# Kernel optimization log

Hardware: AMD Instinct MI355X
Metric: run time of the kernel (lower is better)

Reference implementation:

```python
import jax, jax.numpy as jnp
import numpy as np
import math

B, H, N, DH = 4, 8, 1024, 128
DPT = 4  # point feature dim (<=4 branch: squared-distance map only)

def setup_inputs() -> dict:
    key = jax.random.key(0)
    ks = jax.random.split(key, 10)
    q   = jax.random.normal(ks[0], (B, H, N, DH), jnp.float32)
    k   = jax.random.normal(ks[1], (B, H, N, DH), jnp.float32)
    v   = jax.random.normal(ks[2], (B, H, N, DH), jnp.float32)
    c   = jax.random.normal(ks[3], (B, H, N, 1), jnp.float32)
    d_q = jax.random.normal(ks[4], (B, N, DPT), jnp.float32)
    d_k = jax.random.normal(ks[5], (B, N, DPT), jnp.float32)
    # LazyLinear(1 -> nhead): per-head scalar weight + bias
    w_w = jax.random.normal(ks[6], (H,), jnp.float32) * 0.1
    b_w = jax.random.normal(ks[7], (H,), jnp.float32) * 0.1
    w_b = jax.random.normal(ks[8], (H,), jnp.float32) * 0.1
    b_b = jax.random.normal(ks[9], (H,), jnp.float32) * 0.1
    return {"q": q, "k": k, "v": v, "c": c, "d_q": d_q, "d_k": d_k,
            "w_w": w_w, "b_w": b_w, "w_b": w_b, "b_b": b_b}

def reference(q, k, v, c, d_q, d_k, w_w, b_w, w_b, b_b):
    dh = q.shape[-1]
    # pairwise squared distances on first 3 coords (torch: under no_grad)
    dq3 = d_q[:, :, :3]
    dk3 = d_k[:, :, :3]
    dist = jax.lax.stop_gradient(
        jnp.sum(dq3 ** 2, -1)[:, :, None]
        + jnp.sum(dk3 ** 2, -1)[:, None, :]
        - 2.0 * jnp.einsum('bnd,bmd->bnm', dq3, dk3))  # [B,N,M]
    db = dist[:, None, :, :]  # [B,1,N,M]
    wbc = lambda p: p[None, :, None, None]  # [1,H,1,1]
    # distmap_w = softplus(-(w*dist + b)); distmap_b = w*dist + b (identity acts)
    distmap_w = jax.nn.softplus(-(db * wbc(w_w) + wbc(b_w)))  # [B,H,N,M]
    distmap_b = db * wbc(w_b) + wbc(b_b)                      # [B,H,N,M]
    # scaled dot-product scores per head
    scores = jnp.einsum('bhnd,bhmd->bhnm', q, k) / math.sqrt(dh)
    scores = jax.nn.relu(scores * distmap_w + distmap_b)
    detr = (jnp.sum(scores, -1, keepdims=True)
            + jnp.sum(jax.nn.softplus(c), 2, keepdims=True) + 1e-9)
    scores = scores / detr
    out = jnp.einsum('bhnm,bhmd->bhnd', scores, v)
    return out, scores
```

## Files before the change

### kernel.cpp

```cpp
#include <hip/hip_runtime.h>


typedef __attribute__((ext_vector_type(8))) short short8;
typedef __attribute__((ext_vector_type(4))) float f32x4;

#define OUT_ELEMS 4194304ull
#define WS_K      0ull
#define WS_VT     8388608ull
#define WS_CS     16777216ull

__device__ __forceinline__ unsigned short f2bf(float f) {
    unsigned u = __builtin_bit_cast(unsigned, f);
    u += 0x7FFFu + ((u >> 16) & 1u);
    return (unsigned short)(u >> 16);
}
__device__ __forceinline__ float bf2f(unsigned short u) {
    return __builtin_bit_cast(float, (unsigned)u << 16);
}
__device__ __forceinline__ float softplus(float x) {
    return fmaxf(x, 0.f) + __logf(1.f + __expf(-fabsf(x)));
}
__device__ __forceinline__ unsigned cvt_pk_bf16(float lo, float hi) {
    unsigned r;
    asm("v_cvt_pk_bf16_f32 %0, %1, %2" : "=v"(r) : "v"(lo), "v"(hi));
    return r;
}
__device__ __forceinline__ void gl_lds16(const unsigned short* g, unsigned short* l) {
    __builtin_amdgcn_global_load_lds(
        (const __attribute__((address_space(1))) void*)g,
        (__attribute__((address_space(3))) void*)l, 16, 0, 0);
}

__global__ __launch_bounds__(256) void prep_all(
    const float* __restrict__ k, const float* __restrict__ v, const float* __restrict__ c,
    unsigned short* __restrict__ wsK, unsigned short* __restrict__ wsVt, float* __restrict__ wsCs)
{
    __shared__ unsigned short sT[64 * 132];
    const int blk = blockIdx.x, tid = threadIdx.x;
    if (blk < 512) {
        int t = blk * 256 + tid;
        for (int u = t; u < 524288; u += 131072) {
            float4 a = reinterpret_cast<const float4*>(k)[u * 2];
            float4 b = reinterpret_cast<const float4*>(k)[u * 2 + 1];
            short8 o;
            o[0]=(short)f2bf(a.x); o[1]=(short)f2bf(a.y); o[2]=(short)f2bf(a.z); o[3]=(short)f2bf(a.w);
            o[4]=(short)f2bf(b.x); o[5]=(short)f2bf(b.y); o[6]=(short)f2bf(b.z); o[7]=(short)f2bf(b.w);
            reinterpret_cast<short8*>(wsK)[u] = o;
        }
    } else if (blk < 1024) {
        const int vb = blk - 512;
        const int bh = vb >> 4, m0 = (vb & 15) * 64;
        const float* src = v + ((size_t)bh * 1024 + m0) * 128;
        for (int i = tid; i < 2048; i += 256) {
            int row = i >> 5, c4 = i & 31;
            float4 t = reinterpret_cast<const float4*>(src)[i];
            unsigned long long pk = (unsigned long long)f2bf(t.x)
                                  | ((unsigned long long)f2bf(t.y) << 16)
                                  | ((unsigned long long)f2bf(t.z) << 32)
                                  | ((unsigned long long)f2bf(t.w) << 48);
            *reinterpret_cast<unsigned long long*>(&sT[row * 132 + c4 * 4]) = pk;
        }
        __syncthreads();
        for (int u = tid; u < 2048; u += 256) {
            int dh = u >> 4, ms = u & 15;
            unsigned long long pk = (unsigned long long)sT[(ms*4+0)*132 + dh]
                                  | ((unsigned long long)sT[(ms*4+1)*132 + dh] << 16)
                                  | ((unsigned long long)sT[(ms*4+2)*132 + dh] << 32)
                                  | ((unsigned long long)sT[(ms*4+3)*132 + dh] << 48);
            *reinterpret_cast<unsigned long long*>(&wsVt[((size_t)bh * 128 + dh) * 1024 + m0 + ms * 4]) = pk;
        }
    } else {
        __shared__ float red[4];
        const int bh = blk - 1024;
        float p = 0.f;
        for (int i = tid; i < 1024; i += 256) p += softplus(c[(size_t)bh * 1024 + i]);
        p += __shfl_xor(p, 32, 64); p += __shfl_xor(p, 16, 64); p += __shfl_xor(p, 8, 64);
        p += __shfl_xor(p,  4, 64); p += __shfl_xor(p,  2, 64); p += __shfl_xor(p, 1, 64);
        if ((tid & 63) == 0) red[tid >> 6] = p;
        __syncthreads();
        if (tid == 0) wsCs[bh] = red[0] + red[1] + red[2] + red[3] + 1e-9f;
    }
}

__global__ __launch_bounds__(512, 4) void sam_main(
    const float* __restrict__ q, const float* __restrict__ dqp, const float* __restrict__ dkp,
    const float* __restrict__ w_w, const float* __restrict__ b_w,
    const float* __restrict__ w_b, const float* __restrict__ b_b,
    const unsigned short* __restrict__ wsK, const unsigned short* __restrict__ wsVt,
    const float* __restrict__ wsCs, float* __restrict__ out)
{
    __shared__ __align__(16) unsigned short uSh[16384];
    __shared__ __align__(16) unsigned short sPb[4096];
    __shared__ float s_red[128];
    __shared__ float s_inv[32];

    const int bid  = blockIdx.x;
    const int xcd  = bid & 7;
    const int j    = bid >> 3;
    const int bh   = xcd * 4 + (j >> 5);
    const int n0   = (j & 31) * 32;
    const int b    = bh >> 3;
    const int h    = bh & 7;
    const int tid  = threadIdx.x;
    const int lane = tid & 63;
    const int wave = tid >> 6;
    const int l15  = lane & 15;
    const int quad = lane >> 4;
    const int wr   = wave >> 2;
    const int wc   = wave & 3;
    const int mq   = wc * 16 + l15;
    const int swz3 = l15 & 7;
    const int r0   = wr * 16 + quad * 4;
    const int q4   = (quad & 1) * 4;

    const float ww = w_w[h], bw = b_w[h], wb = w_b[h], bb = b_b[h];
    const float wwn = -ww, bwn = -bw;
    const float SCALE = 0.08838834764831845f;

    const unsigned short* gKbh = wsK  + (size_t)bh * 131072;
    const unsigned short* gVbh = wsVt + (size_t)bh * 131072;
    const int krow  = tid >> 4;
    const int koff0 = krow * 128 + (((tid & 15) ^ (krow & 7)) << 3);
    const int vdh   = tid >> 3;
    const int voff0 = vdh * 1024 + (((tid & 7) ^ (vdh & 7)) << 3);
    const int ldso  = wave * 512;

    auto stageK = [&](int buf, int t) {
        const unsigned short* g = gKbh + t * 8192 + koff0;
        gl_lds16(g,        &uSh[buf * 8192 + ldso]);
        gl_lds16(g + 4096, &uSh[buf * 8192 + 4096 + ldso]);
    };
    auto stageV = [&](int buf, int t) {
        const unsigned short* g = gVbh + t * 64 + voff0;
        gl_lds16(g,         &uSh[buf * 8192 + ldso]);
        gl_lds16(g + 65536, &uSh[buf * 8192 + 4096 + ldso]);
    };

    stageK(1, 0);
    {
        const float* qbase = q + ((size_t)bh * 1024 + n0) * 128;
        for (int i = tid; i < 1024; i += 512) {
            int row = i >> 5, c4 = i & 31;
            float4 t = reinterpret_cast<const float4*>(qbase)[i];
            unsigned long long pk = (unsigned long long)f2bf(t.x * SCALE)
                                  | ((unsigned long long)f2bf(t.y * SCALE) << 16)
                                  | ((unsigned long long)f2bf(t.z * SCALE) << 32)
                                  | ((unsigned long long)f2bf(t.w * SCALE) << 48);
            *reinterpret_cast<unsigned long long*>(&uSh[row * 136 + c4 * 4]) = pk;
        }
    }
    float qxm[4], qym[4], qzm[4], qs[4];
    #pragma unroll
    for (int r = 0; r < 4; r++) {
        float4 d4 = reinterpret_cast<const float4*>(dqp)[(size_t)b * 1024 + n0 + r0 + r];
        qxm[r] = -2.f * d4.x; qym[r] = -2.f * d4.y; qzm[r] = -2.f * d4.z;
        qs[r] = d4.x*d4.x + d4.y*d4.y + d4.z*d4.z;
    }
    const float cs = wsCs[bh];
    __syncthreads();
    short8 afr[4];
    {
        const unsigned short* aq = &uSh[(wr * 16 + l15) * 136 + quad * 8];
        #pragma unroll
        for (int ks = 0; ks < 4; ks++)
            afr[ks] = *reinterpret_cast<const short8*>(aq + ks * 32);
    }
    __syncthreads();

    const float4* dkb = reinterpret_cast<const float4*>(dkp) + (size_t)b * 1024 + mq;

    float rs[4] = {0.f, 0.f, 0.f, 0.f};
    unsigned vreg[16][2];
    #pragma unroll
    for (int t = 0; t < 16; t++) {
        const int bswz = (1 ^ (t & 1)) * 8192;
        if (t < 15) stageK(t & 1, t + 1);
        f32x4 cacc = {0.f, 0.f, 0.f, 0.f};
        const unsigned short* bq = &uSh[bswz + mq * 128];
        #pragma unroll
        for (int ks = 0; ks < 4; ks++) {
            short8 bfr = *reinterpret_cast<const short8*>(bq + (((ks * 4 + quad) ^ swz3) << 3));
            cacc = __builtin_amdgcn_mfma_f32_16x16x32_bf16(afr[ks], bfr, cacc, 0, 0, 0);
        }
        float4 d4 = dkb[t * 64];
        float ksq = d4.x*d4.x + d4.y*d4.y + d4.z*d4.z;
        float val[4];
        #pragma unroll
        for (int r = 0; r < 4; r++) {
            float dist = qs[r] + ksq + qxm[r]*d4.x + qym[r]*d4.y + qzm[r]*d4.z;
            float aw = softplus(dist * wwn + bwn);
            float ab = dist * wb + bb;
            val[r] = fmaxf(cacc[r] * aw + ab, 0.f);
            rs[r] += val[r];
        }
        vreg[t][0] = cvt_pk_bf16(val[0], val[1]);
        vreg[t][1] = cvt_pk_bf16(val[2], val[3]);
        __syncthreads();
    }

    #pragma unroll
    for (int r = 0; r < 4; r++) {
        float ts = rs[r];
        ts += __shfl_xor(ts, 1, 64);
        ts += __shfl_xor(ts, 2, 64);
        ts += __shfl_xor(ts, 4, 64);
        ts += __shfl_xor(ts, 8, 64);
        if (l15 == 0) s_red[wc * 32 + r0 + r] = ts;
    }
    auto sp_write = [&](int buf, unsigned pv0, unsigned pv1) {
        unsigned short* pb = sPb + buf * 2048;
        const int gm = mq >> 3, c7 = mq & 7;
        pb[(r0 + 0) * 64 + (((gm ^ (q4 + 0)) << 3) | c7)] = (unsigned short)(pv0);
        pb[(r0 + 1) * 64 + (((gm ^ (q4 + 1)) << 3) | c7)] = (unsigned short)(pv0 >> 16);
        pb[(r0 + 2) * 64 + (((gm ^ (q4 + 2)) << 3) | c7)] = (unsigned short)(pv1);
        pb[(r0 + 3) * 64 + (((gm ^ (q4 + 3)) << 3) | c7)] = (unsigned short)(pv1 >> 16);
    };
    stageV(0, 0);
    sp_write(0, vreg[0][0], vreg[0][1]);
    __syncthreads();
    if (tid < 32) s_inv[tid] = 1.f / (s_red[tid] + s_red[32 + tid] + s_red[64 + tid] + s_red[96 + tid] + cs);
    __syncthreads();

    float inv4[4];
    #pragma unroll
    for (int r = 0; r < 4; r++) inv4[r] = s_inv[r0 + r];

    f32x4 oacc[2];
    oacc[0] = {0.f, 0.f, 0.f, 0.f};
    oacc[1] = {0.f, 0.f, 0.f, 0.f};
    const int crow = tid >> 4, cc4 = tid & 15;
    const int cidx = crow * 64 + ((((cc4 >> 1) ^ (crow & 7)) << 3) | ((cc4 & 1) << 2));
    float* scrow = out + OUT_ELEMS + ((size_t)bh << 20) + (size_t)(n0 + crow) * 1024 + cc4 * 4;
    const float cinv = s_inv[crow];
    const int prow = wr * 16 + l15;

    #pragma unroll
    for (int t = 0; t < 16; t++) {
        const int bb2 = t & 1;
        if (t < 15) {
            stageV(bb2 ^ 1, t + 1);
            sp_write(bb2 ^ 1, vreg[t + 1][0], vreg[t + 1][1]);
        }
        {
            unsigned long long pk = *reinterpret_cast<const unsigned long long*>(&sPb[bb2 * 2048 + cidx]);
            f32x4 o;
            o[0] = bf2f((unsigned short)(pk      )) * cinv;
            o[1] = bf2f((unsigned short)(pk >> 16)) * cinv;
            o[2] = bf2f((unsigned short)(pk >> 32)) * cinv;
            o[3] = bf2f((unsigned short)(pk >> 48)) * cinv;
            __builtin_nontemporal_store(o, reinterpret_cast<f32x4*>(scrow + t * 64));
        }
        #pragma unroll
        for (int ks2 = 0; ks2 < 2; ks2++) {
            short8 pfr = *reinterpret_cast<const short8*>(
                &sPb[bb2 * 2048 + prow * 64 + (((ks2 * 4 + quad) ^ swz3) << 3)]);
            #pragma unroll
            for (int df = 0; df < 2; df++) {
                const int dh = wc * 32 + df * 16 + l15;
                short8 vfr = *reinterpret_cast<const short8*>(
                    &uSh[bb2 * 8192 + dh * 64 + (((ks2 * 4 + quad) ^ swz3) << 3)]);
                oacc[df] = __builtin_amdgcn_mfma_f32_16x16x32_bf16(pfr, vfr, oacc[df], 0, 0, 0);
            }
        }
        if (t < 15) __syncthreads();
    }

    {
        float* obase = out + ((size_t)bh * 1024 + n0 + r0) * 128 + wc * 32 + l15;
        #pragma unroll
        for (int df = 0; df < 2; df++)
            #pragma unroll
            for (int r = 0; r < 4; r++)
                obase[(size_t)r * 128 + df * 16] = oacc[df][r] * inv4[r];
    }
}

extern "C" void kernel_launch(void* const* d_in, const int* in_sizes, int n_in,
                              void* d_out, int out_size, void* d_ws, size_t ws_size,
                              hipStream_t stream) {
    const float* q   = (const float*)d_in[0];
    const float* k   = (const float*)d_in[1];
    const float* v   = (const float*)d_in[2];
    const float* c   = (const float*)d_in[3];
    const float* dq  = (const float*)d_in[4];
    const float* dk  = (const float*)d_in[5];
    const float* w_w = (const float*)d_in[6];
    const float* b_w = (const float*)d_in[7];
    const float* w_b = (const float*)d_in[8];
    const float* b_b = (const float*)d_in[9];
    float* out = (float*)d_out;
    char* ws = (char*)d_ws;
    unsigned short* wsK  = (unsigned short*)(ws + WS_K);
    unsigned short* wsVt = (unsigned short*)(ws + WS_VT);
    float* wsCs   = (float*)(ws + WS_CS);

    hipLaunchKernelGGL(prep_all, dim3(1056), dim3(256), 0, stream, k, v, c, wsK, wsVt, wsCs);
    hipLaunchKernelGGL(sam_main, dim3(1024), dim3(512), 0, stream,
                       q, dq, dk, w_w, b_w, w_b, b_b, wsK, wsVt, wsCs, out);
}
```

Baseline: 258.3 us.

## Double key/value tile width to 128 columns, halving barriers per pass

The K and V staging tiles now cover 128 key columns per stage instead of 64, and LDS grows to 64 KB for the double buffers. Each barrier therefore covers two MFMA sub-tiles, which halves the syncs in both the score pass and the PV pass. The score row buffer is widened to 128 columns, and the s_red/s_inv scratch now aliases it. The final output is staged through LDS so it can be written with coalesced 32-byte nontemporal stores. The larger LDS footprint may lower the number of blocks resident per CU.

```diff
diff --git a/kernel.cpp b/kernel.cpp
--- a/kernel.cpp
+++ b/kernel.cpp
@@ -89,10 +89,10 @@
     const unsigned short* __restrict__ wsK, const unsigned short* __restrict__ wsVt,
     const float* __restrict__ wsCs, float* __restrict__ out)
 {
-    __shared__ __align__(16) unsigned short uSh[16384];
+    __shared__ __align__(16) unsigned short uSh[32768];
     __shared__ __align__(16) unsigned short sPb[4096];
-    __shared__ float s_red[128];
-    __shared__ float s_inv[32];
+    float* s_red = reinterpret_cast<float*>(sPb);
+    float* s_inv = s_red + 128;
 
     const int bid  = blockIdx.x;
     const int xcd  = bid & 7;
@@ -119,21 +119,22 @@
 
     const unsigned short* gKbh = wsK  + (size_t)bh * 131072;
     const unsigned short* gVbh = wsVt + (size_t)bh * 131072;
-    const int krow  = tid >> 4;
-    const int koff0 = krow * 128 + (((tid & 15) ^ (krow & 7)) << 3);
-    const int vdh   = tid >> 3;
-    const int voff0 = vdh * 1024 + (((tid & 7) ^ (vdh & 7)) << 3);
-    const int ldso  = wave * 512;
-
-    auto stageK = [&](int buf, int t) {
-        const unsigned short* g = gKbh + t * 8192 + koff0;
-        gl_lds16(g,        &uSh[buf * 8192 + ldso]);
-        gl_lds16(g + 4096, &uSh[buf * 8192 + 4096 + ldso]);
+    const int srow  = tid >> 4;
+    const int koff0 = srow * 128  + (((tid & 15) ^ (srow & 7)) << 3);
+    const int voff0 = srow * 1024 + (((tid & 15) ^ (srow & 7)) << 3);
+    const int ldsoW = wave * 512;
+
+    auto stageK = [&](int buf, int c) {
+        const unsigned short* g = gKbh + c * 16384 + koff0;
+        #pragma unroll
+        for (int i = 0; i < 4; i++)
+            gl_lds16(g + i * 4096, &uSh[buf * 16384 + ldsoW + i * 4096]);
     };
-    auto stageV = [&](int buf, int t) {
-        const unsigned short* g = gVbh + t * 64 + voff0;
-        gl_lds16(g,         &uSh[buf * 8192 + ldso]);
-        gl_lds16(g + 65536, &uSh[buf * 8192 + 4096 + ldso]);
+    auto stageV = [&](int buf, int c) {
+        const unsigned short* g = gVbh + c * 128 + voff0;
+        #pragma unroll
+        for (int i = 0; i < 4; i++)
+            gl_lds16(g + i * 32768, &uSh[buf * 16384 + ldsoW + i * 4096]);
     };
 
     stageK(1, 0);
@@ -172,32 +173,37 @@
     float rs[4] = {0.f, 0.f, 0.f, 0.f};
     unsigned vreg[16][2];
     #pragma unroll
-    for (int t = 0; t < 16; t++) {
-        const int bswz = (1 ^ (t & 1)) * 8192;
-        if (t < 15) stageK(t & 1, t + 1);
-        f32x4 cacc = {0.f, 0.f, 0.f, 0.f};
-        const unsigned short* bq = &uSh[bswz + mq * 128];
-        #pragma unroll
-        for (int ks = 0; ks < 4; ks++) {
-            short8 bfr = *reinterpret_cast<const short8*>(bq + (((ks * 4 + quad) ^ swz3) << 3));
-            cacc = __builtin_amdgcn_mfma_f32_16x16x32_bf16(afr[ks], bfr, cacc, 0, 0, 0);
-        }
-        float4 d4 = dkb[t * 64];
-        float ksq = d4.x*d4.x + d4.y*d4.y + d4.z*d4.z;
-        float val[4];
-        #pragma unroll
-        for (int r = 0; r < 4; r++) {
-            float dist = qs[r] + ksq + qxm[r]*d4.x + qym[r]*d4.y + qzm[r]*d4.z;
-            float aw = softplus(dist * wwn + bwn);
-            float ab = dist * wb + bb;
-            val[r] = fmaxf(cacc[r] * aw + ab, 0.f);
-            rs[r] += val[r];
-        }
-        vreg[t][0] = cvt_pk_bf16(val[0], val[1]);
-        vreg[t][1] = cvt_pk_bf16(val[2], val[3]);
-        __syncthreads();
-    }
-
+    for (int c = 0; c < 8; c++) {
+        const int rbuf = ((c & 1) ^ 1) * 16384;
+        if (c < 7) stageK(c & 1, c + 1);
+        #pragma unroll
+        for (int tt = 0; tt < 2; tt++) {
+            const int t = c * 2 + tt;
+            f32x4 cacc = {0.f, 0.f, 0.f, 0.f};
+            const unsigned short* bq = &uSh[rbuf + (tt * 64 + mq) * 128];
+            #pragma unroll
+            for (int ks = 0; ks < 4; ks++) {
+                short8 bfr = *reinterpret_cast<const short8*>(bq + (((ks * 4 + quad) ^ swz3) << 3));
+                cacc = __builtin_amdgcn_mfma_f32_16x16x32_bf16(afr[ks], bfr, cacc, 0, 0, 0);
+            }
+            float4 d4 = dkb[t * 64];
+            float ksq = d4.x*d4.x + d4.y*d4.y + d4.z*d4.z;
+            float val[4];
+            #pragma unroll
+            for (int r = 0; r < 4; r++) {
+                float dist = qs[r] + ksq + qxm[r]*d4.x + qym[r]*d4.y + qzm[r]*d4.z;
+                float aw = softplus(dist * wwn + bwn);
+                float ab = dist * wb + bb;
+                val[r] = fmaxf(cacc[r] * aw + ab, 0.f);
+                rs[r] += val[r];
+            }
+            vreg[t][0] = cvt_pk_bf16(val[0], val[1]);
+            vreg[t][1] = cvt_pk_bf16(val[2], val[3]);
+        }
+        __syncthreads();
+    }
+
+    stageV(0, 0);
     #pragma unroll
     for (int r = 0; r < 4; r++) {
         float ts = rs[r];
@@ -207,71 +213,87 @@
         ts += __shfl_xor(ts, 8, 64);
         if (l15 == 0) s_red[wc * 32 + r0 + r] = ts;
     }
-    auto sp_write = [&](int buf, unsigned pv0, unsigned pv1) {
-        unsigned short* pb = sPb + buf * 2048;
-        const int gm = mq >> 3, c7 = mq & 7;
-        pb[(r0 + 0) * 64 + (((gm ^ (q4 + 0)) << 3) | c7)] = (unsigned short)(pv0);
-        pb[(r0 + 1) * 64 + (((gm ^ (q4 + 1)) << 3) | c7)] = (unsigned short)(pv0 >> 16);
-        pb[(r0 + 2) * 64 + (((gm ^ (q4 + 2)) << 3) | c7)] = (unsigned short)(pv1);
-        pb[(r0 + 3) * 64 + (((gm ^ (q4 + 3)) << 3) | c7)] = (unsigned short)(pv1 >> 16);
-    };
-    stageV(0, 0);
-    sp_write(0, vreg[0][0], vreg[0][1]);
     __syncthreads();
     if (tid < 32) s_inv[tid] = 1.f / (s_red[tid] + s_red[32 + tid] + s_red[64 + tid] + s_red[96 + tid] + cs);
     __syncthreads();
-
     float inv4[4];
     #pragma unroll
     for (int r = 0; r < 4; r++) inv4[r] = s_inv[r0 + r];
+    const int crow = tid >> 4, cc4 = tid & 15;
+    const float cinv = s_inv[crow];
+    __syncthreads();
 
     f32x4 oacc[2];
     oacc[0] = {0.f, 0.f, 0.f, 0.f};
     oacc[1] = {0.f, 0.f, 0.f, 0.f};
-    const int crow = tid >> 4, cc4 = tid & 15;
-    const int cidx = crow * 64 + ((((cc4 >> 1) ^ (crow & 7)) << 3) | ((cc4 & 1) << 2));
-    float* scrow = out + OUT_ELEMS + ((size_t)bh << 20) + (size_t)(n0 + crow) * 1024 + cc4 * 4;
-    const float cinv = s_inv[crow];
+    float* scrow = out + OUT_ELEMS + ((size_t)bh << 20) + (size_t)(n0 + crow) * 1024 + cc4 * 8;
     const int prow = wr * 16 + l15;
-
-    #pragma unroll
-    for (int t = 0; t < 16; t++) {
-        const int bb2 = t & 1;
-        if (t < 15) {
-            stageV(bb2 ^ 1, t + 1);
-            sp_write(bb2 ^ 1, vreg[t + 1][0], vreg[t + 1][1]);
-        }
+    const int gm = mq >> 3, c7 = mq & 7;
+
+    #pragma unroll
+    for (int c = 0; c < 8; c++) {
+        const int vbuf = (c & 1) * 16384;
         {
-            unsigned long long pk = *reinterpret_cast<const unsigned long long*>(&sPb[bb2 * 2048 + cidx]);
-            f32x4 o;
-            o[0] = bf2f((unsigned short)(pk      )) * cinv;
-            o[1] = bf2f((unsigned short)(pk >> 16)) * cinv;
-            o[2] = bf2f((unsigned short)(pk >> 32)) * cinv;
-            o[3] = bf2f((unsigned short)(pk >> 48)) * cinv;
-            __builtin_nontemporal_store(o, reinterpret_cast<f32x4*>(scrow + t * 64));
-        }
-        #pragma unroll
-        for (int ks2 = 0; ks2 < 2; ks2++) {
-            short8 pfr = *reinterpret_cast<const short8*>(
-                &sPb[bb2 * 2048 + prow * 64 + (((ks2 * 4 + quad) ^ swz3) << 3)]);
+            unsigned a0 = vreg[c*2][0],   a1 = vreg[c*2][1];
+            unsigned b0 = vreg[c*2+1][0], b1 = vreg[c*2+1][1];
+            sPb[(r0+0)*128 + ((( gm      ^ (q4+0)) << 3) | c7)] = (unsigned short)a0;
+            sPb[(r0+1)*128 + ((( gm      ^ (q4+1)) << 3) | c7)] = (unsigned short)(a0 >> 16);
+            sPb[(r0+2)*128 + ((( gm      ^ (q4+2)) << 3) | c7)] = (unsigned short)a1;
+            sPb[(r0+3)*128 + ((( gm      ^ (q4+3)) << 3) | c7)] = (unsigned short)(a1 >> 16);
+            sPb[(r0+0)*128 + ((((8|gm)   ^ (q4+0)) << 3) | c7)] = (unsigned short)b0;
+            sPb[(r0+1)*128 + ((((8|gm)   ^ (q4+1)) << 3) | c7)] = (unsigned short)(b0 >> 16);
+            sPb[(r0+2)*128 + ((((8|gm)   ^ (q4+2)) << 3) | c7)] = (unsigned short)b1;
+            sPb[(r0+3)*128 + ((((8|gm)   ^ (q4+3)) << 3) | c7)] = (unsigned short)(b1 >> 16);
+        }
+        __syncthreads();
+        if (c < 7) stageV((c & 1) ^ 1, c + 1);
+        {
+            short8 pk8 = *reinterpret_cast<const short8*>(&sPb[crow * 128 + ((cc4 ^ (crow & 7)) << 3)]);
+            f32x4 o1, o2;
+            o1[0] = bf2f((unsigned short)pk8[0]) * cinv;
+            o1[1] = bf2f((unsigned short)pk8[1]) * cinv;
+            o1[2] = bf2f((unsigned short)pk8[2]) * cinv;
+            o1[3] = bf2f((unsigned short)pk8[3]) * cinv;
+            o2[0] = bf2f((unsigned short)pk8[4]) * cinv;
+            o2[1] = bf2f((unsigned short)pk8[5]) * cinv;
+            o2[2] = bf2f((unsigned short)pk8[6]) * cinv;
+            o2[3] = bf2f((unsigned short)pk8[7]) * cinv;
+            __builtin_nontemporal_store(o1, reinterpret_cast<f32x4*>(scrow + c * 128));
+            __builtin_nontemporal_store(o2, reinterpret_cast<f32x4*>(scrow + c * 128 + 4));
+        }
+        #pragma unroll
+        for (int tt = 0; tt < 2; tt++) {
             #pragma unroll
-            for (int df = 0; df < 2; df++) {
-                const int dh = wc * 32 + df * 16 + l15;
-                short8 vfr = *reinterpret_cast<const short8*>(
-                    &uSh[bb2 * 8192 + dh * 64 + (((ks2 * 4 + quad) ^ swz3) << 3)]);
-                oacc[df] = __builtin_amdgcn_mfma_f32_16x16x32_bf16(pfr, vfr, oacc[df], 0, 0, 0);
+            for (int ks2 = 0; ks2 < 2; ks2++) {
+                const int gP = tt * 8 + ks2 * 4 + quad;
+                short8 pfr = *reinterpret_cast<const short8*>(
+                    &sPb[prow * 128 + ((gP ^ (prow & 7)) << 3)]);
+                #pragma unroll
+                for (int df = 0; df < 2; df++) {
+                    const int dh = wc * 32 + df * 16 + l15;
+                    short8 vfr = *reinterpret_cast<const short8*>(
+                        &uSh[vbuf + dh * 128 + ((gP ^ swz3) << 3)]);
+                    oacc[df] = __builtin_amdgcn_mfma_f32_16x16x32_bf16(pfr, vfr, oacc[df], 0, 0, 0);
+                }
             }
         }
-        if (t < 15) __syncthreads();
+        __syncthreads();
     }
 
     {
-        float* obase = out + ((size_t)bh * 1024 + n0 + r0) * 128 + wc * 32 + l15;
+        float* sO = reinterpret_cast<float*>(uSh);
         #pragma unroll
         for (int df = 0; df < 2; df++)
             #pragma unroll
             for (int r = 0; r < 4; r++)
-                obase[(size_t)r * 128 + df * 16] = oacc[df][r] * inv4[r];
+                sO[(r0 + r) * 136 + wc * 32 + df * 16 + l15] = oacc[df][r] * inv4[r];
+        __syncthreads();
+        const float* src = &sO[crow * 136 + cc4 * 8];
+        f32x4 a = *reinterpret_cast<const f32x4*>(src);
+        f32x4 d = *reinterpret_cast<const f32x4*>(src + 4);
+        float* obase = out + ((size_t)bh * 1024 + n0 + crow) * 128 + cc4 * 8;
+        __builtin_nontemporal_store(a, reinterpret_cast<f32x4*>(obase));
+        __builtin_nontemporal_store(d, reinterpret_cast<f32x4*>(obase + 4));
     }
 }
 
```

After: 263.7 us. 2.1% more time.

## Stage K in larger 128-row chunks and coalesce output stores via LDS

Applied to the files above, without the earlier changes.

Each K staging step now loads two 64-row tiles at once into a doubled LDS buffer, which halves the number of barriers in the score loop. The final output is first written to LDS and then stored to global memory as contiguous 32-byte nontemporal vectors per thread instead of scattered scalar stores. LDS use per block doubles, which may cut how many blocks can be resident per CU.

```diff
diff --git a/kernel.cpp b/kernel.cpp
--- a/kernel.cpp
+++ b/kernel.cpp
@@ -89,7 +89,7 @@
     const unsigned short* __restrict__ wsK, const unsigned short* __restrict__ wsVt,
     const float* __restrict__ wsCs, float* __restrict__ out)
 {
-    __shared__ __align__(16) unsigned short uSh[16384];
+    __shared__ __align__(16) unsigned short uSh[32768];
     __shared__ __align__(16) unsigned short sPb[4096];
     __shared__ float s_red[128];
     __shared__ float s_inv[32];
@@ -119,21 +119,22 @@
 
     const unsigned short* gKbh = wsK  + (size_t)bh * 131072;
     const unsigned short* gVbh = wsVt + (size_t)bh * 131072;
-    const int krow  = tid >> 4;
-    const int koff0 = krow * 128 + (((tid & 15) ^ (krow & 7)) << 3);
-    const int vdh   = tid >> 3;
-    const int voff0 = vdh * 1024 + (((tid & 7) ^ (vdh & 7)) << 3);
-    const int ldso  = wave * 512;
-
-    auto stageK = [&](int buf, int t) {
-        const unsigned short* g = gKbh + t * 8192 + koff0;
-        gl_lds16(g,        &uSh[buf * 8192 + ldso]);
-        gl_lds16(g + 4096, &uSh[buf * 8192 + 4096 + ldso]);
+    const int srow   = tid >> 4;
+    const int koff0  = srow * 128 + (((tid & 15) ^ (srow & 7)) << 3);
+    const int vdh    = tid >> 3;
+    const int voff0  = vdh * 1024 + (((tid & 7) ^ (vdh & 7)) << 3);
+    const int ldsoW  = wave * 512;
+
+    auto stageK = [&](int buf, int c) {
+        const unsigned short* g = gKbh + c * 16384 + koff0;
+        #pragma unroll
+        for (int i = 0; i < 4; i++)
+            gl_lds16(g + i * 4096, &uSh[buf * 16384 + ldsoW + i * 4096]);
     };
     auto stageV = [&](int buf, int t) {
         const unsigned short* g = gVbh + t * 64 + voff0;
-        gl_lds16(g,         &uSh[buf * 8192 + ldso]);
-        gl_lds16(g + 65536, &uSh[buf * 8192 + 4096 + ldso]);
+        gl_lds16(g,         &uSh[buf * 8192 + ldsoW]);
+        gl_lds16(g + 65536, &uSh[buf * 8192 + 4096 + ldsoW]);
     };
 
     stageK(1, 0);
@@ -172,29 +173,33 @@
     float rs[4] = {0.f, 0.f, 0.f, 0.f};
     unsigned vreg[16][2];
     #pragma unroll
-    for (int t = 0; t < 16; t++) {
-        const int bswz = (1 ^ (t & 1)) * 8192;
-        if (t < 15) stageK(t & 1, t + 1);
-        f32x4 cacc = {0.f, 0.f, 0.f, 0.f};
-        const unsigned short* bq = &uSh[bswz + mq * 128];
-        #pragma unroll
-        for (int ks = 0; ks < 4; ks++) {
-            short8 bfr = *reinterpret_cast<const short8*>(bq + (((ks * 4 + quad) ^ swz3) << 3));
-            cacc = __builtin_amdgcn_mfma_f32_16x16x32_bf16(afr[ks], bfr, cacc, 0, 0, 0);
-        }
-        float4 d4 = dkb[t * 64];
-        float ksq = d4.x*d4.x + d4.y*d4.y + d4.z*d4.z;
-        float val[4];
-        #pragma unroll
-        for (int r = 0; r < 4; r++) {
-            float dist = qs[r] + ksq + qxm[r]*d4.x + qym[r]*d4.y + qzm[r]*d4.z;
-            float aw = softplus(dist * wwn + bwn);
-            float ab = dist * wb + bb;
-            val[r] = fmaxf(cacc[r] * aw + ab, 0.f);
-            rs[r] += val[r];
-        }
-        vreg[t][0] = cvt_pk_bf16(val[0], val[1]);
-        vreg[t][1] = cvt_pk_bf16(val[2], val[3]);
+    for (int c = 0; c < 8; c++) {
+        const int rbuf = ((c & 1) ^ 1) * 16384;
+        if (c < 7) stageK(c & 1, c + 1);
+        #pragma unroll
+        for (int tt = 0; tt < 2; tt++) {
+            const int t = c * 2 + tt;
+            f32x4 cacc = {0.f, 0.f, 0.f, 0.f};
+            const unsigned short* bq = &uSh[rbuf + (tt * 64 + mq) * 128];
+            #pragma unroll
+            for (int ks = 0; ks < 4; ks++) {
+                short8 bfr = *reinterpret_cast<const short8*>(bq + (((ks * 4 + quad) ^ swz3) << 3));
+                cacc = __builtin_amdgcn_mfma_f32_16x16x32_bf16(afr[ks], bfr, cacc, 0, 0, 0);
+            }
+            float4 d4 = dkb[t * 64];
+            float ksq = d4.x*d4.x + d4.y*d4.y + d4.z*d4.z;
+            float val[4];
+            #pragma unroll
+            for (int r = 0; r < 4; r++) {
+                float dist = qs[r] + ksq + qxm[r]*d4.x + qym[r]*d4.y + qzm[r]*d4.z;
+                float aw = softplus(dist * wwn + bwn);
+                float ab = dist * wb + bb;
+                val[r] = fmaxf(cacc[r] * aw + ab, 0.f);
+                rs[r] += val[r];
+            }
+            vreg[t][0] = cvt_pk_bf16(val[0], val[1]);
+            vreg[t][1] = cvt_pk_bf16(val[2], val[3]);
+        }
         __syncthreads();
     }
 
@@ -266,12 +271,20 @@
     }
 
     {
-        float* obase = out + ((size_t)bh * 1024 + n0 + r0) * 128 + wc * 32 + l15;
+        __syncthreads();
+        float* sO = reinterpret_cast<float*>(uSh);
         #pragma unroll
         for (int df = 0; df < 2; df++)
             #pragma unroll
             for (int r = 0; r < 4; r++)
-                obase[(size_t)r * 128 + df * 16] = oacc[df][r] * inv4[r];
+                sO[(r0 + r) * 136 + wc * 32 + df * 16 + l15] = oacc[df][r] * inv4[r];
+        __syncthreads();
+        const float* src = &sO[crow * 136 + cc4 * 8];
+        f32x4 a = *reinterpret_cast<const f32x4*>(src);
+        f32x4 d = *reinterpret_cast<const f32x4*>(src + 4);
+        float* obase = out + ((size_t)bh * 1024 + n0 + crow) * 128 + cc4 * 8;
+        __builtin_nontemporal_store(a, reinterpret_cast<f32x4*>(obase));
+        __builtin_nontemporal_store(d, reinterpret_cast<f32x4*>(obase + 4));
     }
 }
 
```

Measured after the change: 258.9 us. About the same (+0.2%).

## Triple-buffer K/V staging with partial vmcnt barriers and cache d_k in LDS

Applied to the files above, without the earlier changes.

Moves K and V tile staging from double to triple buffering, so two tiles are in flight at once. The full __syncthreads are replaced by s_waitcnt vmcnt(N) barriers that only wait for the oldest outstanding loads. The key-point coordinates and their squared norms are also precomputed once into LDS, replacing a per-iteration global float4 load and the norm computation. This raises LDS use per block, which may lower occupancy under launch_bounds(512,4), and the hand-counted vmcnt values must match the issued load counts exactly, including the nontemporal stores.

```diff
diff --git a/kernel.cpp b/kernel.cpp
--- a/kernel.cpp
+++ b/kernel.cpp
@@ -8,6 +8,9 @@
 #define WS_K      0ull
 #define WS_VT     8388608ull
 #define WS_CS     16777216ull
+
+#define CBAR(N) asm volatile("s_waitcnt vmcnt(" #N ") lgkmcnt(0)\n\ts_barrier" ::: "memory")
+#define LBAR()  asm volatile("s_waitcnt lgkmcnt(0)\n\ts_barrier" ::: "memory")
 
 __device__ __forceinline__ unsigned short f2bf(float f) {
     unsigned u = __builtin_bit_cast(unsigned, f);
@@ -89,7 +92,8 @@
     const unsigned short* __restrict__ wsK, const unsigned short* __restrict__ wsVt,
     const float* __restrict__ wsCs, float* __restrict__ out)
 {
-    __shared__ __align__(16) unsigned short uSh[16384];
+    __shared__ __align__(16) unsigned short uSh[24576];
+    __shared__ __align__(16) float sdkf[4096];
     __shared__ __align__(16) unsigned short sPb[4096];
     __shared__ float s_red[128];
     __shared__ float s_inv[32];
@@ -123,20 +127,19 @@
     const int koff0 = krow * 128 + (((tid & 15) ^ (krow & 7)) << 3);
     const int vdh   = tid >> 3;
     const int voff0 = vdh * 1024 + (((tid & 7) ^ (vdh & 7)) << 3);
-    const int ldso  = wave * 512;
+    const int ldsoW = wave * 512;
 
     auto stageK = [&](int buf, int t) {
         const unsigned short* g = gKbh + t * 8192 + koff0;
-        gl_lds16(g,        &uSh[buf * 8192 + ldso]);
-        gl_lds16(g + 4096, &uSh[buf * 8192 + 4096 + ldso]);
+        gl_lds16(g,        &uSh[buf * 8192 + ldsoW]);
+        gl_lds16(g + 4096, &uSh[buf * 8192 + 4096 + ldsoW]);
     };
     auto stageV = [&](int buf, int t) {
         const unsigned short* g = gVbh + t * 64 + voff0;
-        gl_lds16(g,         &uSh[buf * 8192 + ldso]);
-        gl_lds16(g + 65536, &uSh[buf * 8192 + 4096 + ldso]);
+        gl_lds16(g,         &uSh[buf * 8192 + ldsoW]);
+        gl_lds16(g + 65536, &uSh[buf * 8192 + 4096 + ldsoW]);
     };
 
-    stageK(1, 0);
     {
         const float* qbase = q + ((size_t)bh * 1024 + n0) * 128;
         for (int i = tid; i < 1024; i += 512) {
@@ -148,6 +151,15 @@
                                   | ((unsigned long long)f2bf(t.w * SCALE) << 48);
             *reinterpret_cast<unsigned long long*>(&uSh[row * 136 + c4 * 4]) = pk;
         }
+        #pragma unroll
+        for (int i = 0; i < 2; i++) {
+            int m = tid + i * 512;
+            float4 d4 = reinterpret_cast<const float4*>(dkp)[(size_t)b * 1024 + m];
+            f32x4 e;
+            e[0] = d4.x; e[1] = d4.y; e[2] = d4.z;
+            e[3] = d4.x*d4.x + d4.y*d4.y + d4.z*d4.z;
+            *reinterpret_cast<f32x4*>(&sdkf[m * 4]) = e;
+        }
     }
     float qxm[4], qym[4], qzm[4], qs[4];
     #pragma unroll
@@ -166,28 +178,27 @@
             afr[ks] = *reinterpret_cast<const short8*>(aq + ks * 32);
     }
     __syncthreads();
-
-    const float4* dkb = reinterpret_cast<const float4*>(dkp) + (size_t)b * 1024 + mq;
+    stageK(0, 0);
+    stageK(1, 1);
+    CBAR(2);
 
     float rs[4] = {0.f, 0.f, 0.f, 0.f};
     unsigned vreg[16][2];
     #pragma unroll
     for (int t = 0; t < 16; t++) {
-        const int bswz = (1 ^ (t & 1)) * 8192;
-        if (t < 15) stageK(t & 1, t + 1);
+        if (t < 14) stageK((t + 2) % 3, t + 2);
         f32x4 cacc = {0.f, 0.f, 0.f, 0.f};
-        const unsigned short* bq = &uSh[bswz + mq * 128];
+        const unsigned short* bq = &uSh[(t % 3) * 8192 + mq * 128];
         #pragma unroll
         for (int ks = 0; ks < 4; ks++) {
             short8 bfr = *reinterpret_cast<const short8*>(bq + (((ks * 4 + quad) ^ swz3) << 3));
             cacc = __builtin_amdgcn_mfma_f32_16x16x32_bf16(afr[ks], bfr, cacc, 0, 0, 0);
         }
-        float4 d4 = dkb[t * 64];
-        float ksq = d4.x*d4.x + d4.y*d4.y + d4.z*d4.z;
+        f32x4 dk4 = *reinterpret_cast<const f32x4*>(&sdkf[(t * 64 + mq) * 4]);
         float val[4];
         #pragma unroll
         for (int r = 0; r < 4; r++) {
-            float dist = qs[r] + ksq + qxm[r]*d4.x + qym[r]*d4.y + qzm[r]*d4.z;
+            float dist = qs[r] + dk4[3] + qxm[r]*dk4[0] + qym[r]*dk4[1] + qzm[r]*dk4[2];
             float aw = softplus(dist * wwn + bwn);
             float ab = dist * wb + bb;
             val[r] = fmaxf(cacc[r] * aw + ab, 0.f);
@@ -195,7 +206,9 @@
         }
         vreg[t][0] = cvt_pk_bf16(val[0], val[1]);
         vreg[t][1] = cvt_pk_bf16(val[2], val[3]);
-        __syncthreads();
+        if (t < 14)      CBAR(2);
+        else if (t == 14) CBAR(0);
+        else              __syncthreads();
     }
 
     #pragma unroll
@@ -216,10 +229,11 @@
         pb[(r0 + 3) * 64 + (((gm ^ (q4 + 3)) << 3) | c7)] = (unsigned short)(pv1 >> 16);
     };
     stageV(0, 0);
+    stageV(1, 1);
     sp_write(0, vreg[0][0], vreg[0][1]);
-    __syncthreads();
+    CBAR(2);
     if (tid < 32) s_inv[tid] = 1.f / (s_red[tid] + s_red[32 + tid] + s_red[64 + tid] + s_red[96 + tid] + cs);
-    __syncthreads();
+    LBAR();
 
     float inv4[4];
     #pragma unroll
@@ -237,10 +251,6 @@
     #pragma unroll
     for (int t = 0; t < 16; t++) {
         const int bb2 = t & 1;
-        if (t < 15) {
-            stageV(bb2 ^ 1, t + 1);
-            sp_write(bb2 ^ 1, vreg[t + 1][0], vreg[t + 1][1]);
-        }
         {
             unsigned long long pk = *reinterpret_cast<const unsigned long long*>(&sPb[bb2 * 2048 + cidx]);
             f32x4 o;
@@ -250,6 +260,8 @@
             o[3] = bf2f((unsigned short)(pk >> 48)) * cinv;
             __builtin_nontemporal_store(o, reinterpret_cast<f32x4*>(scrow + t * 64));
         }
+        if (t < 14) stageV((t + 2) % 3, t + 2);
+        if (t < 15) sp_write(bb2 ^ 1, vreg[t + 1][0], vreg[t + 1][1]);
         #pragma unroll
         for (int ks2 = 0; ks2 < 2; ks2++) {
             short8 pfr = *reinterpret_cast<const short8*>(
@@ -258,11 +270,12 @@
             for (int df = 0; df < 2; df++) {
                 const int dh = wc * 32 + df * 16 + l15;
                 short8 vfr = *reinterpret_cast<const short8*>(
-                    &uSh[bb2 * 8192 + dh * 64 + (((ks2 * 4 + quad) ^ swz3) << 3)]);
+                    &uSh[(t % 3) * 8192 + dh * 64 + (((ks2 * 4 + quad) ^ swz3) << 3)]);
                 oacc[df] = __builtin_amdgcn_mfma_f32_16x16x32_bf16(pfr, vfr, oacc[df], 0, 0, 0);
             }
         }
-        if (t < 15) __syncthreads();
+        if (t < 14)      CBAR(3);
+        else if (t == 14) CBAR(1);
     }
 
     {
```

Result: no change. 254.8 us (-1.4%).
